# Kernel optimization log

Measured on AMD Instinct MI355X. Metric: run time of the kernel, lower is better.

## Reference

```python
import jax, jax.numpy as jnp
import numpy as np

K, N = 4096, 4096
GROUP_SIZE = 128
N_GROUPS = N // GROUP_SIZE  # 32
BATCH, SEQ = 4, 2048
NBITS = 4


def setup_inputs() -> dict:
    key = jax.random.key(0)
    ks = jax.random.split(key, 7)
    x = jax.random.normal(ks[0], (BATCH, SEQ, N), dtype=jnp.float32)
    W_q = jax.random.randint(ks[1], (K, N), 0, 2 ** NBITS, dtype=jnp.int32)
    scales = jax.random.uniform(ks[2], (K, N_GROUPS, 1), dtype=jnp.float32) * 0.05 + 0.001
    zeros = jax.random.uniform(ks[3], (K, N_GROUPS, 1), dtype=jnp.float32) * (2 ** NBITS)
    mu1 = jax.random.uniform(ks[4], (N,), dtype=jnp.float32) + 0.5  # per-column sinkhorn factor
    mu2 = jax.random.uniform(ks[5], (K,), dtype=jnp.float32) + 0.5  # per-row sinkhorn factor
    bias = jax.random.normal(ks[6], (K,), dtype=jnp.float32)
    return {"x": x, "W_q": W_q, "scales": scales, "zeros": zeros,
            "mu1": mu1, "mu2": mu2, "bias": bias}


def reference(x, W_q, scales, zeros, mu1, mu2, bias):
    input_dtype = x.dtype
    n_groups = scales.shape[1]
    group_size = W_q.shape[1] // n_groups
    # group-wise dequant: [K, n_groups, group_size]
    Q_g = W_q.astype(jnp.float32).reshape(K, n_groups, group_size)
    W_deq_norm = (Q_g - zeros) * scales
    # undo sinkhorn row/col normalization
    W_deq = W_deq_norm.reshape(K, N) * mu2[:, None] * mu1[None, :]
    W_deq = W_deq.astype(input_dtype)
    # linear: x [B,S,N] @ W_deq.T [N,K] + bias [K]
    return jnp.einsum('bsn,kn->bsk', x, W_deq) + bias
```

## Files before the change

### kernel.cpp

```cpp
#include <hip/hip_runtime.h>
#include <hip/hip_bf16.h>
#include <stdint.h>

#define M_DIM 8192
#define N_C   4096
#define K_OUT 4096
#define NGRP  32

typedef __attribute__((ext_vector_type(8))) short bf16x8;
typedef __attribute__((ext_vector_type(4))) float f32x4;

__device__ __forceinline__ unsigned short f2b(float f) {
  unsigned u = __float_as_uint(f);
  return (unsigned short)((u + 0x7fffu + ((u >> 16) & 1u)) >> 16);
}

__device__ __forceinline__ void gload_lds16(const void* g, void* l) {
  __builtin_amdgcn_global_load_lds(
      (const __attribute__((address_space(1))) void*)g,
      (__attribute__((address_space(3))) void*)l,
      16, 0, 0);
}

__global__ void convert_x_kernel(const float* __restrict__ x,
                                 unsigned short* __restrict__ xb) {
  const int total = (M_DIM * N_C) / 8;
  const int stride = gridDim.x * blockDim.x;
  for (int i = blockIdx.x * blockDim.x + threadIdx.x; i < total; i += stride) {
    const float4* p = (const float4*)(x + (size_t)i * 8);
    float4 a = p[0];
    float4 b = p[1];
    union { unsigned short u[8]; uint4 v; } o;
    o.u[0] = f2b(a.x); o.u[1] = f2b(a.y); o.u[2] = f2b(a.z); o.u[3] = f2b(a.w);
    o.u[4] = f2b(b.x); o.u[5] = f2b(b.y); o.u[6] = f2b(b.z); o.u[7] = f2b(b.w);
    *(uint4*)(xb + (size_t)i * 8) = o.v;
  }
}

__global__ void dequant_w_kernel(const int* __restrict__ Wq,
                                 const float* __restrict__ scales,
                                 const float* __restrict__ zeros,
                                 const float* __restrict__ mu1,
                                 const float* __restrict__ mu2,
                                 unsigned short* __restrict__ wb) {
  const int total = (K_OUT * N_C) / 8;
  const int stride = gridDim.x * blockDim.x;
  for (int i = blockIdx.x * blockDim.x + threadIdx.x; i < total; i += stride) {
    const int k  = i >> 9;
    const int nc = (i & 511) << 3;
    const int g  = nc >> 7;
    const float s = scales[k * NGRP + g];
    const float z = zeros[k * NGRP + g];
    const float f  = s * mu2[k];
    const float zf = z * f;
    const int4* q4 = (const int4*)(Wq + (size_t)k * N_C + nc);
    int4 q0 = q4[0], q1 = q4[1];
    const float4* m4 = (const float4*)(mu1 + nc);
    float4 m0 = m4[0], m1 = m4[1];
    union { unsigned short u[8]; uint4 v; } o;
    o.u[0] = f2b(((float)q0.x * f - zf) * m0.x);
    o.u[1] = f2b(((float)q0.y * f - zf) * m0.y);
    o.u[2] = f2b(((float)q0.z * f - zf) * m0.z);
    o.u[3] = f2b(((float)q0.w * f - zf) * m0.w);
    o.u[4] = f2b(((float)q1.x * f - zf) * m1.x);
    o.u[5] = f2b(((float)q1.y * f - zf) * m1.y);
    o.u[6] = f2b(((float)q1.z * f - zf) * m1.z);
    o.u[7] = f2b(((float)q1.w * f - zf) * m1.w);
    *(uint4*)(wb + (size_t)i * 8) = o.v;
  }
}

__global__ __launch_bounds__(256, 2) void gemm_bf16_kernel(
    const unsigned short* __restrict__ Xb,
    const unsigned short* __restrict__ Wb,
    const float* __restrict__ bias,
    float* __restrict__ out) {
  __shared__ unsigned short sA[128 * 64];
  __shared__ unsigned short sB[128 * 64];

  const int k0 = blockIdx.x * 128;
  const int m0 = blockIdx.y * 128;
  const int t = threadIdx.x;
  const int wv = t >> 6;
  const int lane = t & 63;
  const int wr = wv >> 1;
  const int wc = wv & 1;

  f32x4 acc[4][4] = {};

  const int soff = wv * 1024 + lane * 16;

  for (int nk = 0; nk < N_C; nk += 64) {
    __syncthreads();
#pragma unroll
    for (int r = 0; r < 4; ++r) {
      const int off  = r * 4096 + soff;
      const int row  = off >> 7;
      const int colb = off & 127;
      gload_lds16((const char*)Xb + (size_t)(m0 + row) * (N_C * 2) + (size_t)nk * 2 + colb,
                  (char*)sA + r * 4096 + wv * 1024);
      gload_lds16((const char*)Wb + (size_t)(k0 + row) * (N_C * 2) + (size_t)nk * 2 + colb,
                  (char*)sB + r * 4096 + wv * 1024);
    }
    __syncthreads();

#pragma unroll
    for (int kk = 0; kk < 2; ++kk) {
      const int col = kk * 32 + (lane >> 4) * 8;
      bf16x8 af[4], bfr[4];
#pragma unroll
      for (int i = 0; i < 4; ++i) {
        const int ra = wr * 64 + i * 16 + (lane & 15);
        af[i] = *(const bf16x8*)(sA + ra * 64 + col);
        const int rb = wc * 64 + i * 16 + (lane & 15);
        bfr[i] = *(const bf16x8*)(sB + rb * 64 + col);
      }
#pragma unroll
      for (int i = 0; i < 4; ++i)
#pragma unroll
        for (int j = 0; j < 4; ++j)
          acc[i][j] = __builtin_amdgcn_mfma_f32_16x16x32_bf16(af[i], bfr[j], acc[i][j], 0, 0, 0);
    }
  }

#pragma unroll
  for (int i = 0; i < 4; ++i) {
    const int mrow = m0 + wr * 64 + i * 16 + (lane >> 4) * 4;
#pragma unroll
    for (int j = 0; j < 4; ++j) {
      const int kc = k0 + wc * 64 + j * 16 + (lane & 15);
      const float b = bias[kc];
#pragma unroll
      for (int r = 0; r < 4; ++r) {
        out[(size_t)(mrow + r) * K_OUT + kc] = acc[i][j][r] + b;
      }
    }
  }
}

extern "C" void kernel_launch(void* const* d_in, const int* in_sizes, int n_in,
                              void* d_out, int out_size, void* d_ws, size_t ws_size,
                              hipStream_t stream) {
  const float* x      = (const float*)d_in[0];
  const int*   Wq     = (const int*)d_in[1];
  const float* scales = (const float*)d_in[2];
  const float* zeros  = (const float*)d_in[3];
  const float* mu1    = (const float*)d_in[4];
  const float* mu2    = (const float*)d_in[5];
  const float* bias   = (const float*)d_in[6];
  float* out = (float*)d_out;

  unsigned short* xb = (unsigned short*)d_ws;
  unsigned short* wb = xb + (size_t)M_DIM * N_C;

  convert_x_kernel<<<2048, 256, 0, stream>>>(x, xb);
  dequant_w_kernel<<<2048, 256, 0, stream>>>(Wq, scales, zeros, mu1, mu2, wb);

  dim3 grid(K_OUT / 128, M_DIM / 128);
  gemm_bf16_kernel<<<grid, 256, 0, stream>>>(xb, wb, bias, out);
}
```

Measured before the change: 364.3 us.

## Rewrite GEMM with 256x256 tiles, 4-stage LDS pipeline, swizzled layout

Replaces the 128x128 single-buffered GEMM with a 256x256 tile per 512-thread block. It uses a 4-deep ring of 32-column K stages in LDS, loaded asynchronously with vmcnt waits so global loads overlap MFMA work. An XOR swizzle on the LDS layout is meant to avoid bank conflicts, the block index is remapped for cache locality, and setprio is raised around the MFMA loop. Each wave holds 8x4 accumulator tiles, so register pressure rises, and the 128 KB of LDS limits residency to one block per CU.

Result: faster. 298.1 us (-18.2%).

```diff
diff --git a/kernel.cpp b/kernel.cpp
--- a/kernel.cpp
+++ b/kernel.cpp
@@ -6,6 +6,7 @@
 #define N_C   4096
 #define K_OUT 4096
 #define NGRP  32
+#define NT    (N_C / 32)
 
 typedef __attribute__((ext_vector_type(8))) short bf16x8;
 typedef __attribute__((ext_vector_type(4))) float f32x4;
@@ -70,70 +71,102 @@
   }
 }
 
-__global__ __launch_bounds__(256, 2) void gemm_bf16_kernel(
+__global__ __launch_bounds__(512) void gemm_bf16_kernel(
     const unsigned short* __restrict__ Xb,
     const unsigned short* __restrict__ Wb,
     const float* __restrict__ bias,
     float* __restrict__ out) {
-  __shared__ unsigned short sA[128 * 64];
-  __shared__ unsigned short sB[128 * 64];
+  __shared__ unsigned short smem[65536];
 
-  const int k0 = blockIdx.x * 128;
-  const int m0 = blockIdx.y * 128;
-  const int t = threadIdx.x;
-  const int wv = t >> 6;
-  const int lane = t & 63;
-  const int wr = wv >> 1;
-  const int wc = wv & 1;
+  const int bid = blockIdx.x;
+  const int swz = (bid & 7) * 64 + (bid >> 3);
+  const int n0 = (swz & 15) * 256;
+  const int m0 = (swz >> 4) * 256;
 
-  f32x4 acc[4][4] = {};
+  const int tid = threadIdx.x;
+  const int w   = tid >> 6;
+  const int l   = tid & 63;
+  const int wr  = w >> 2;
+  const int wc  = w & 3;
 
-  const int soff = wv * 1024 + lane * 16;
+  const char* Xc = (const char*)Xb;
+  const char* Wc = (const char*)Wb;
+  const char* srcA[2];
+  const char* srcB[2];
+  int dstOff[2];
+#pragma unroll
+  for (int e = 0; e < 2; ++e) {
+    const int P  = (e * 8 + w) * 1024 + l * 16;
+    const int r  = P >> 6;
+    const int sl = ((P >> 4) & 3) ^ ((r >> 1) & 3);
+    srcA[e] = Xc + (size_t)(m0 + r) * (N_C * 2) + sl * 16;
+    srcB[e] = Wc + (size_t)(n0 + r) * (N_C * 2) + sl * 16;
+    dstOff[e] = (e * 8 + w) * 1024;
+  }
 
-  for (int nk = 0; nk < N_C; nk += 64) {
-    __syncthreads();
+  int offa[8], offb[4];
 #pragma unroll
-    for (int r = 0; r < 4; ++r) {
-      const int off  = r * 4096 + soff;
-      const int row  = off >> 7;
-      const int colb = off & 127;
-      gload_lds16((const char*)Xb + (size_t)(m0 + row) * (N_C * 2) + (size_t)nk * 2 + colb,
-                  (char*)sA + r * 4096 + wv * 1024);
-      gload_lds16((const char*)Wb + (size_t)(k0 + row) * (N_C * 2) + (size_t)nk * 2 + colb,
-                  (char*)sB + r * 4096 + wv * 1024);
-    }
-    __syncthreads();
+  for (int i = 0; i < 8; ++i) {
+    const int r  = wr * 128 + i * 16 + (l & 15);
+    const int sl = (l >> 4) ^ ((r >> 1) & 3);
+    offa[i] = (r * 64 + sl * 16) >> 1;
+  }
+#pragma unroll
+  for (int j = 0; j < 4; ++j) {
+    const int r  = wc * 64 + j * 16 + (l & 15);
+    const int sl = (l >> 4) ^ ((r >> 1) & 3);
+    offb[j] = (16384 + r * 64 + sl * 16) >> 1;
+  }
+
+  f32x4 acc[8][4] = {};
+  char* ldsc = (char*)smem;
+
+#define STAGE(tt)                                                            \
+  { const int sb = ((tt) & 3) * 32768; const size_t ko = (size_t)(tt) * 64;  \
+    gload_lds16(srcA[0] + ko, ldsc + sb + dstOff[0]);                        \
+    gload_lds16(srcA[1] + ko, ldsc + sb + dstOff[1]);                        \
+    gload_lds16(srcB[0] + ko, ldsc + sb + 16384 + dstOff[0]);                \
+    gload_lds16(srcB[1] + ko, ldsc + sb + 16384 + dstOff[1]); }
+
+  STAGE(0)
+  STAGE(1)
+  STAGE(2)
+
+#define KSTEP(VMSTR, tt, DOSTAGE)                                            \
+  { asm volatile("s_waitcnt vmcnt(" VMSTR ")\n\ts_barrier" ::: "memory");    \
+    const int bufo = ((tt) & 3) * 16384;                                     \
+    bf16x8 af[8]; bf16x8 bfv[4];                                             \
+    _Pragma("unroll") for (int i = 0; i < 8; ++i)                            \
+      af[i] = *(const bf16x8*)(smem + bufo + offa[i]);                       \
+    _Pragma("unroll") for (int j = 0; j < 4; ++j)                            \
+      bfv[j] = *(const bf16x8*)(smem + bufo + offb[j]);                      \
+    if (DOSTAGE) STAGE((tt) + 3)                                             \
+    __builtin_amdgcn_s_setprio(1);                                           \
+    _Pragma("unroll") for (int i = 0; i < 8; ++i)                            \
+      _Pragma("unroll") for (int j = 0; j < 4; ++j)                          \
+        acc[i][j] = __builtin_amdgcn_mfma_f32_16x16x32_bf16(af[i], bfv[j],   \
+                                                            acc[i][j], 0, 0, 0); \
+    __builtin_amdgcn_s_setprio(0); }
+
+#pragma unroll 1
+  for (int kt = 0; kt < NT - 3; ++kt) KSTEP("8", kt, 1)
+  KSTEP("8", NT - 3, 0)
+  KSTEP("4", NT - 2, 0)
+  KSTEP("0", NT - 1, 0)
+
+#undef KSTEP
+#undef STAGE
 
 #pragma unroll
-    for (int kk = 0; kk < 2; ++kk) {
-      const int col = kk * 32 + (lane >> 4) * 8;
-      bf16x8 af[4], bfr[4];
+  for (int j = 0; j < 4; ++j) {
+    const int col = n0 + wc * 64 + j * 16 + (l & 15);
+    const float bv = bias[col];
 #pragma unroll
-      for (int i = 0; i < 4; ++i) {
-        const int ra = wr * 64 + i * 16 + (lane & 15);
-        af[i] = *(const bf16x8*)(sA + ra * 64 + col);
-        const int rb = wc * 64 + i * 16 + (lane & 15);
-        bfr[i] = *(const bf16x8*)(sB + rb * 64 + col);
-      }
+    for (int i = 0; i < 8; ++i) {
+      const int row = m0 + wr * 128 + i * 16 + (l >> 4) * 4;
 #pragma unroll
-      for (int i = 0; i < 4; ++i)
-#pragma unroll
-        for (int j = 0; j < 4; ++j)
-          acc[i][j] = __builtin_amdgcn_mfma_f32_16x16x32_bf16(af[i], bfr[j], acc[i][j], 0, 0, 0);
-    }
-  }
-
-#pragma unroll
-  for (int i = 0; i < 4; ++i) {
-    const int mrow = m0 + wr * 64 + i * 16 + (lane >> 4) * 4;
-#pragma unroll
-    for (int j = 0; j < 4; ++j) {
-      const int kc = k0 + wc * 64 + j * 16 + (lane & 15);
-      const float b = bias[kc];
-#pragma unroll
-      for (int r = 0; r < 4; ++r) {
-        out[(size_t)(mrow + r) * K_OUT + kc] = acc[i][j][r] + b;
-      }
+      for (int rr = 0; rr < 4; ++rr)
+        out[(size_t)(row + rr) * K_OUT + col] = acc[i][j][rr] + bv;
     }
   }
 }
@@ -156,6 +189,6 @@
   convert_x_kernel<<<2048, 256, 0, stream>>>(x, xb);
   dequant_w_kernel<<<2048, 256, 0, stream>>>(Wq, scales, zeros, mu1, mu2, wb);
 
-  dim3 grid(K_OUT / 128, M_DIM / 128);
-  gemm_bf16_kernel<<<grid, 256, 0, stream>>>(xb, wb, bias, out);
+  dim3 grid((M_DIM / 256) * (K_OUT / 256));
+  gemm_bf16_kernel<<<grid, 512, 0, stream>>>(xb, wb, bias, out);
 }
```
